# Kernel optimization log

Hardware: AMD Instinct MI355X
Metric: run time of the kernel (lower is better)

## Reference

```python
import jax, jax.numpy as jnp
import numpy as np

N_NODES = 50000
N_EDGES = 800000
IN_CH, HID, HEADS, OUT_CH = 16, 64, 4, 8
NEG_SLOPE = 0.2


def _add_self_loops(edge_index, num_nodes):
    loop = jnp.arange(num_nodes, dtype=edge_index.dtype)
    loops = jnp.stack([loop, loop])  # [2, N]
    return jnp.concatenate([edge_index, loops], axis=1)


def _gat_conv(x, src, dst, W, a_src, a_dst, bias, concat):
    """PyG-style GATConv: linear -> per-edge LeakyReLU attention -> segment
    softmax over incoming edges -> scatter-add aggregate."""
    N = x.shape[0]
    H, C = a_src.shape
    h = (x @ W).reshape(N, H, C)                      # [N,H,C]
    alpha_src = (h * a_src).sum(-1)                   # [N,H]
    alpha_dst = (h * a_dst).sum(-1)                   # [N,H]
    e = jax.nn.leaky_relu(alpha_src[src] + alpha_dst[dst], NEG_SLOPE)  # [E,H]
    # numerically stable segment softmax over edges grouped by dst
    e_max = jax.ops.segment_max(e, dst, num_segments=N)
    e_exp = jnp.exp(e - e_max[dst])
    denom = jax.ops.segment_sum(e_exp, dst, num_segments=N)
    alpha = e_exp / denom[dst]                        # [E,H]
    msg = h[src] * alpha[:, :, None]                  # [E,H,C]
    out = jax.ops.segment_sum(msg, dst, num_segments=N)  # [N,H,C]
    if concat:
        return out.reshape(N, H * C) + bias
    return out.mean(axis=1) + bias


def setup_inputs() -> dict:
    key = jax.random.key(0)
    ks = jax.random.split(key, 12)
    s = 0.1
    return {
        "x": jax.random.normal(ks[0], (N_NODES, IN_CH), jnp.float32),
        "edge_index": jax.random.randint(ks[1], (2, N_EDGES), 0, N_NODES, jnp.int64),
        "W1": jax.random.normal(ks[2], (IN_CH, HEADS * HID), jnp.float32) * s,
        "as1": jax.random.normal(ks[3], (HEADS, HID), jnp.float32) * s,
        "ad1": jax.random.normal(ks[4], (HEADS, HID), jnp.float32) * s,
        "b1": jnp.zeros((HEADS * HID,), jnp.float32),
        "W2": jax.random.normal(ks[5], (HEADS * HID, HEADS * HID), jnp.float32) * s,
        "as2": jax.random.normal(ks[6], (HEADS, HID), jnp.float32) * s,
        "ad2": jax.random.normal(ks[7], (HEADS, HID), jnp.float32) * s,
        "b2": jnp.zeros((HID,), jnp.float32),
        "Wc": jax.random.normal(ks[8], (HID, OUT_CH), jnp.float32) * s,
        "bc": jnp.zeros((OUT_CH,), jnp.float32),
    }


def reference(x, edge_index, W1, as1, ad1, b1, W2, as2, ad2, b2, Wc, bc):
    ei = _add_self_loops(edge_index, x.shape[0])
    src, dst = ei[0], ei[1]
    h = _gat_conv(x, src, dst, W1, as1, ad1, b1, concat=True)
    h = jax.nn.elu(h)
    h = _gat_conv(h, src, dst, W2, as2, ad2, b2, concat=False)
    h = jax.nn.elu(h)
    return h @ Wc + bc  # [N, OUT_CH]
```

## Files before the change

kernel.cpp:

```cpp
#include <hip/hip_runtime.h>
#include <math.h>

#define NODES   50000
#define HEADS   4
#define HID     64
#define FDIM    256
#define IN_CH   16
#define NEG_SLOPE 0.2f

typedef unsigned short ushort_t;
typedef unsigned int uint_t;
typedef __attribute__((ext_vector_type(8))) short bf16x8;
typedef __attribute__((ext_vector_type(4))) float f32x4;
typedef __attribute__((ext_vector_type(2))) float f32x2;

__device__ inline ushort_t f2bf(float f) {
    uint_t u = __float_as_uint(f);
    u += 0x7fffu + ((u >> 16) & 1u);
    return (ushort_t)(u >> 16);
}
__device__ inline uint_t f2h(float f) {
    _Float16 h = (_Float16)f;
    return (uint_t)*(ushort_t*)&h;
}
__device__ inline float h2f(uint_t u) {
    ushort_t us = (ushort_t)u;
    _Float16 h = *(_Float16*)&us;
    return (float)h;
}


__global__ __launch_bounds__(256) void k_prep(const float* __restrict__ x,
                                              const float* __restrict__ W1,
                                              const float* __restrict__ as1,
                                              const float* __restrict__ ad1,
                                              const float* __restrict__ W2,
                                              const int* __restrict__ ei, int E,
                                              ushort_t* __restrict__ h,
                                              float* __restrict__ asrc,
                                              float* __restrict__ adst,
                                              ushort_t* __restrict__ W2T,
                                              int* __restrict__ deg, int Nn, int NB) {
    int bid = blockIdx.x, t = threadIdx.x;
    if (bid >= NB + 256) {
        int e = (bid - NB - 256) * 256 + t;
        int Etot = E + Nn;
        if (e >= Etot) return;
        int d = (e < E) ? ei[E + e] : (e - E);
        if (d >= 0 && d < Nn) atomicAdd(&deg[d], 1);
        return;
    }
    if (bid >= NB) {
        int idx = (bid - NB) * 256 + t;
        int n = idx >> 8, k = idx & 255;
        W2T[idx] = f2bf(W2[k * FDIM + n]);
        return;
    }
    float w1c[16];
#pragma unroll
    for (int k = 0; k < 16; ++k) w1c[k] = W1[k * FDIM + t];
    float av = as1[t], dv = ad1[t];
    int hh = t >> 6;
#pragma unroll
    for (int j = 0; j < 8; ++j) {
        int n = bid * 8 + j;
        if (n >= Nn) break;
        const float4* xp = (const float4*)(x + n * IN_CH);
        float4 x0 = xp[0], x1 = xp[1], x2 = xp[2], x3 = xp[3];
        float s = x0.x * w1c[0]  + x0.y * w1c[1]  + x0.z * w1c[2]  + x0.w * w1c[3]
                + x1.x * w1c[4]  + x1.y * w1c[5]  + x1.z * w1c[6]  + x1.w * w1c[7]
                + x2.x * w1c[8]  + x2.y * w1c[9]  + x2.z * w1c[10] + x2.w * w1c[11]
                + x3.x * w1c[12] + x3.y * w1c[13] + x3.z * w1c[14] + x3.w * w1c[15];
        uint_t pv = (uint_t)f2bf(s);
        uint_t ov = __shfl_down(pv, 1);
        if (!(t & 1)) *(uint_t*)(h + (long)n * FDIM + t) = pv | (ov << 16);
        float p1 = s * av, p2 = s * dv;
#pragma unroll
        for (int off = 1; off < 64; off <<= 1) {
            p1 += __shfl_xor(p1, off);
            p2 += __shfl_xor(p2, off);
        }
        if ((t & 63) == 0) {
            asrc[n * 4 + hh] = p1;
            adst[n * 4 + hh] = p2;
        }
    }
}


__global__ __launch_bounds__(256) void k_scanA(const int* __restrict__ deg,
                                               int* __restrict__ bsum, int N) {
    __shared__ int sh[256];
    int t = threadIdx.x;
    int i0 = blockIdx.x * 4096 + t * 16;
    int s = 0;
#pragma unroll
    for (int j = 0; j < 16; ++j) s += (i0 + j < N) ? deg[i0 + j] : 0;
    sh[t] = s;
    __syncthreads();
    for (int off = 128; off; off >>= 1) {
        if (t < off) sh[t] += sh[t + off];
        __syncthreads();
    }
    if (t == 0) bsum[blockIdx.x] = sh[0];
}

__global__ void k_scanB(int* __restrict__ bsum, int* __restrict__ rowst, int nb, int N) {
    int t = threadIdx.x;
    int orig = (t < nb) ? bsum[t] : 0;
    int v = orig;
#pragma unroll
    for (int off = 1; off < 64; off <<= 1) {
        int u = __shfl_up(v, off);
        if (t >= off) v += u;
    }
    if (t < nb) bsum[t] = v - orig;
    if (t == 63) rowst[N] = v;
}

__global__ __launch_bounds__(256) void k_scanC(const int* __restrict__ deg,
                                               const int* __restrict__ bsum,
                                               int* __restrict__ rowst,
                                               int* __restrict__ cursor, int N) {
    __shared__ int sh[256];
    int t = threadIdx.x, b = blockIdx.x;
    int i0 = b * 4096 + t * 16;
    int v[16], s = 0;
#pragma unroll
    for (int j = 0; j < 16; ++j) { v[j] = (i0 + j < N) ? deg[i0 + j] : 0; s += v[j]; }
    sh[t] = s;
    __syncthreads();
    for (int off = 1; off < 256; off <<= 1) {
        int u = (t >= off) ? sh[t - off] : 0;
        __syncthreads();
        sh[t] += u;
        __syncthreads();
    }
    int excl = sh[t] - s + bsum[b];
#pragma unroll
    for (int j = 0; j < 16; ++j) {
        if (i0 + j < N) { rowst[i0 + j] = excl; cursor[i0 + j] = excl; }
        excl += v[j];
    }
}

__global__ void k_scatter(const int* __restrict__ ei, int E, int N,
                          int* __restrict__ cursor, int2* __restrict__ csr2) {
    int e = blockIdx.x * blockDim.x + threadIdx.x;
    int Etot = E + N;
    if (e >= Etot) return;
    int s, d;
    if (e < E) { s = ei[e]; d = ei[E + e]; } else { s = d = e - E; }
    if (d < 0 || d >= N) return;
    int pos = atomicAdd(&cursor[d], 1);
    csr2[pos] = make_int2(s, d);
}


__global__ __launch_bounds__(256) void k_gemm2(const ushort_t* __restrict__ A,
                                               const ushort_t* __restrict__ BT,
                                               const float* __restrict__ as2,
                                               const float* __restrict__ ad2,
                                               ushort_t* __restrict__ C,
                                               float* __restrict__ asrc,
                                               float* __restrict__ adst, int M) {
    __shared__ short As[64 * 40];
    __shared__ short Bs[64 * 40];
    __shared__ float2 red[64][2];
    int tid = threadIdx.x;
    int row0 = blockIdx.y * 64, col0 = blockIdx.x * 64;
    int wid = tid >> 6, lane = tid & 63;
    int wm = wid >> 1, wn = wid & 1;
    int quad = lane >> 4, lm = lane & 15;
    int lr = tid >> 2, lk = (tid & 3) * 8;
    f32x4 acc[2][2] = {};
    for (int k0 = 0; k0 < FDIM; k0 += 32) {
        uint4 av = {0u, 0u, 0u, 0u};
        int ar = row0 + lr;
        if (ar < M) av = *(const uint4*)(A + (long)ar * FDIM + k0 + lk);
        *(uint4*)(&As[lr * 40 + lk]) = av;
        uint4 bv = *(const uint4*)(BT + (long)(col0 + lr) * FDIM + k0 + lk);
        *(uint4*)(&Bs[lr * 40 + lk]) = bv;
        __syncthreads();
        bf16x8 a0 = *(const bf16x8*)(&As[(wm * 32 + lm) * 40 + quad * 8]);
        bf16x8 a1 = *(const bf16x8*)(&As[(wm * 32 + 16 + lm) * 40 + quad * 8]);
        bf16x8 b0 = *(const bf16x8*)(&Bs[(wn * 32 + lm) * 40 + quad * 8]);
        bf16x8 b1 = *(const bf16x8*)(&Bs[(wn * 32 + 16 + lm) * 40 + quad * 8]);
        acc[0][0] = __builtin_amdgcn_mfma_f32_16x16x32_bf16(a0, b0, acc[0][0], 0, 0, 0);
        acc[0][1] = __builtin_amdgcn_mfma_f32_16x16x32_bf16(a0, b1, acc[0][1], 0, 0, 0);
        acc[1][0] = __builtin_amdgcn_mfma_f32_16x16x32_bf16(a1, b0, acc[1][0], 0, 0, 0);
        acc[1][1] = __builtin_amdgcn_mfma_f32_16x16x32_bf16(a1, b1, acc[1][1], 0, 0, 0);
        __syncthreads();
    }
#pragma unroll
    for (int mi = 0; mi < 2; ++mi)
#pragma unroll
        for (int ni = 0; ni < 2; ++ni)
#pragma unroll
            for (int r = 0; r < 4; ++r) {
                int row = row0 + wm * 32 + mi * 16 + quad * 4 + r;
                int col = col0 + wn * 32 + ni * 16 + lm;
                if (row < M) C[(long)row * FDIM + col] = f2bf(acc[mi][ni][r]);
            }
    float asv0 = as2[col0 + wn * 32 + lm], asv1 = as2[col0 + wn * 32 + 16 + lm];
    float adv0 = ad2[col0 + wn * 32 + lm], adv1 = ad2[col0 + wn * 32 + 16 + lm];
#pragma unroll
    for (int mi = 0; mi < 2; ++mi)
#pragma unroll
        for (int r = 0; r < 4; ++r) {
            float ps = acc[mi][0][r] * asv0 + acc[mi][1][r] * asv1;
            float pd = acc[mi][0][r] * adv0 + acc[mi][1][r] * adv1;
#pragma unroll
            for (int off = 1; off < 16; off <<= 1) {
                ps += __shfl_xor(ps, off);
                pd += __shfl_xor(pd, off);
            }
            if (lm == 0) red[wm * 32 + mi * 16 + quad * 4 + r][wn] = make_float2(ps, pd);
        }
    __syncthreads();
    if (tid < 64) {
        int row = row0 + tid;
        if (row < M) {
            float2 e0 = red[tid][0], e1 = red[tid][1];
            asrc[row * 4 + blockIdx.x] = e0.x + e1.x;
            adst[row * 4 + blockIdx.x] = e0.y + e1.y;
        }
    }
}


__global__ void k_pw(const int2* __restrict__ csr2, const float* __restrict__ asrc,
                     const float* __restrict__ adst, uint_t* __restrict__ pwb, int Etot) {
    int e = blockIdx.x * blockDim.x + threadIdx.x;
    if (e >= Etot) return;
    int2 sd = csr2[e];
    float4 av = *(const float4*)(asrc + sd.x * 4);
    float4 dv = *(const float4*)(adst + sd.y * 4);
    float t[4] = {av.x + dv.x, av.y + dv.y, av.z + dv.z, av.w + dv.w};
    uint_t sh = (uint_t)sd.x << 16;
#pragma unroll
    for (int h = 0; h < 4; ++h) {
        float tt = (t[h] > 0.f) ? t[h] : NEG_SLOPE * t[h];
        pwb[h * Etot + e] = sh | f2h(__expf(tt));
    }
}


__device__ inline void fma8(f32x2& a0, f32x2& a1, f32x2& a2, f32x2& a3,
                            uint4 hv, float pw) {
    f32x2 p = {pw, pw};
    f32x2 u;
    u.x = __uint_as_float(hv.x << 16); u.y = __uint_as_float(hv.x & 0xffff0000u);
    a0 += p * u;
    u.x = __uint_as_float(hv.y << 16); u.y = __uint_as_float(hv.y & 0xffff0000u);
    a1 += p * u;
    u.x = __uint_as_float(hv.z << 16); u.y = __uint_as_float(hv.z & 0xffff0000u);
    a2 += p * u;
    u.x = __uint_as_float(hv.w << 16); u.y = __uint_as_float(hv.w & 0xffff0000u);
    a3 += p * u;
}

__global__ __launch_bounds__(256) void k_agg(const ushort_t* __restrict__ h,
                                             const uint_t* __restrict__ pwb,
                                             const int* __restrict__ row_start,
                                             const float* __restrict__ b1,
                                             const float* __restrict__ b2,
                                             const float* __restrict__ Wc,
                                             const float* __restrict__ bc,
                                             ushort_t* __restrict__ hout,
                                             float* __restrict__ fout,
                                             int mode, int Etot, int N) {
    __shared__ float zsh[2 * FDIM];
    __shared__ float wsh[584];
    int tid  = threadIdx.x;
    int hh   = tid >> 6;
    int lane = tid & 63;
    int half = lane >> 5;
    int l32  = lane & 31;
    int g    = l32 >> 3;
    int cg   = l32 & 7;
    int d    = blockIdx.x * 2 + half;
    bool valid = d < N;

    if (!mode) {
        for (int i = tid; i < 584; i += 256)
            wsh[i] = (i < 512) ? Wc[i] : ((i < 520) ? bc[i - 512] : b2[i - 520]);
    }

    int s0 = 0, s1 = 0;
    if (valid) { s0 = row_start[d]; s1 = row_start[d + 1]; }
    int cnt  = s1 - s0;
    int maxc = max(cnt, __shfl_xor(cnt, 32));
    const uint_t* pwp = pwb + (long)hh * Etot;
    const char* hbase = (const char*)h + (hh * HID + cg * 8) * 2;

    f32x2 a0 = {0.f, 0.f}, a1 = {0.f, 0.f}, a2 = {0.f, 0.f}, a3 = {0.f, 0.f};
    float den = 0.f;

    for (int off = 0; off < maxc; off += 16) {
        int i0 = s0 + off + g;
        uint_t u0 = (i0      < s1) ? pwp[i0]      : 0u;
        uint_t u1 = (i0 + 4  < s1) ? pwp[i0 + 4]  : 0u;
        uint_t u2 = (i0 + 8  < s1) ? pwp[i0 + 8]  : 0u;
        uint_t u3 = (i0 + 12 < s1) ? pwp[i0 + 12] : 0u;
        uint4 hv0 = *(const uint4*)(hbase + ((size_t)(u0 >> 16) << 9));
        uint4 hv1 = *(const uint4*)(hbase + ((size_t)(u1 >> 16) << 9));
        uint4 hv2 = *(const uint4*)(hbase + ((size_t)(u2 >> 16) << 9));
        uint4 hv3 = *(const uint4*)(hbase + ((size_t)(u3 >> 16) << 9));
        float pw0 = h2f(u0 & 0xffffu), pw1 = h2f(u1 & 0xffffu);
        float pw2 = h2f(u2 & 0xffffu), pw3 = h2f(u3 & 0xffffu);
        den += (pw0 + pw1) + (pw2 + pw3);
        fma8(a0, a1, a2, a3, hv0, pw0);
        fma8(a0, a1, a2, a3, hv1, pw1);
        fma8(a0, a1, a2, a3, hv2, pw2);
        fma8(a0, a1, a2, a3, hv3, pw3);
    }
#pragma unroll
    for (int off = 8; off <= 16; off <<= 1) {
        a0.x += __shfl_xor(a0.x, off); a0.y += __shfl_xor(a0.y, off);
        a1.x += __shfl_xor(a1.x, off); a1.y += __shfl_xor(a1.y, off);
        a2.x += __shfl_xor(a2.x, off); a2.y += __shfl_xor(a2.y, off);
        a3.x += __shfl_xor(a3.x, off); a3.y += __shfl_xor(a3.y, off);
        den  += __shfl_xor(den, off);
    }

    if (mode) {
        if (g == 0 && valid) {
            float inv = 1.f / den;
            float v[8] = {a0.x, a0.y, a1.x, a1.y, a2.x, a2.y, a3.x, a3.y};
            const float* bp = b1 + hh * HID + cg * 8;
#pragma unroll
            for (int j = 0; j < 8; ++j) {
                float t = v[j] * inv + bp[j];
                v[j] = (t > 0.f) ? t : __expf(t) - 1.f;
            }
            uint4 u;
            u.x = (uint_t)f2bf(v[0]) | ((uint_t)f2bf(v[1]) << 16);
            u.y = (uint_t)f2bf(v[2]) | ((uint_t)f2bf(v[3]) << 16);
            u.z = (uint_t)f2bf(v[4]) | ((uint_t)f2bf(v[5]) << 16);
            u.w = (uint_t)f2bf(v[6]) | ((uint_t)f2bf(v[7]) << 16);
            *(uint4*)(hout + (long)d * FDIM + hh * HID + cg * 8) = u;
        }
    } else {
        if (g == 0 && valid) {
            float inv = 1.f / den;
            float v[8] = {a0.x, a0.y, a1.x, a1.y, a2.x, a2.y, a3.x, a3.y};
            int zb = half * FDIM + hh * HID + cg * 8;
#pragma unroll
            for (int j = 0; j < 8; ++j) zsh[zb + j] = v[j] * inv;
        }
        __syncthreads();
        if (tid < 128) {
            int node = tid >> 6, c = tid & 63;
            int dd = blockIdx.x * 2 + node;
            if (dd < N) {
                const float* zp = zsh + node * FDIM;
                float zv = 0.25f * (zp[c] + zp[64 + c] + zp[128 + c] + zp[192 + c])
                         + wsh[520 + c];
                zv = (zv > 0.f) ? zv : __expf(zv) - 1.f;
                zsh[node * FDIM + c] = zv;
            }
        }
        __syncthreads();
        if (tid < 16) {
            int node = tid >> 3, o = tid & 7;
            int dd = blockIdx.x * 2 + node;
            if (dd < N) {
                float acc = wsh[512 + o];
                const float* zp = zsh + node * FDIM;
#pragma unroll 8
                for (int c = 0; c < 64; ++c) acc += zp[c] * wsh[c * 8 + o];
                fout[(long)dd * 8 + o] = acc;
            }
        }
    }
}


extern "C" void kernel_launch(void* const* d_in, const int* in_sizes, int n_in,
                              void* d_out, int out_size, void* d_ws, size_t ws_size,
                              hipStream_t stream) {
    const float* x   = (const float*)d_in[0];
    const int*   ei  = (const int*)d_in[1];
    const float* W1  = (const float*)d_in[2];
    const float* as1 = (const float*)d_in[3];
    const float* ad1 = (const float*)d_in[4];
    const float* b1  = (const float*)d_in[5];
    const float* W2  = (const float*)d_in[6];
    const float* as2 = (const float*)d_in[7];
    const float* ad2 = (const float*)d_in[8];
    const float* b2  = (const float*)d_in[9];
    const float* Wc  = (const float*)d_in[10];
    const float* bc  = (const float*)d_in[11];
    float* out = (float*)d_out;

    const int N = NODES;
    const int E = in_sizes[1] / 2;
    const int Etot = E + N;

    char* ws = (char*)d_ws;
    size_t off = 0;
    auto alloc = [&](size_t bytes) {
        void* p = ws + off;
        off = (off + bytes + 255) & ~(size_t)255;
        return p;
    };
    ushort_t* hbf    = (ushort_t*)alloc((size_t)N * FDIM * 2);
    ushort_t* hact   = (ushort_t*)alloc((size_t)N * FDIM * 2);
    float*    asrc   = (float*)alloc((size_t)N * HEADS * 4);
    float*    adst   = (float*)alloc((size_t)N * HEADS * 4);
    ushort_t* W2T    = (ushort_t*)alloc((size_t)FDIM * FDIM * 2);
    int*      deg    = (int*)alloc((size_t)N * 4);
    int*      rowst  = (int*)alloc((size_t)(N + 1) * 4);
    int*      cursor = (int*)alloc((size_t)N * 4);
    int*      bsum   = (int*)alloc(64 * 4);
    int2*     csr2   = (int2*)alloc((size_t)Etot * 8);
    uint_t*   pwb    = (uint_t*)alloc((size_t)Etot * HEADS * 4);

    const int tpb = 256;
    int egrid = (Etot + tpb - 1) / tpb;
    int nb = (N + 4095) / 4096;
    int NB = (N + 7) / 8;

    hipMemsetAsync(deg, 0, (size_t)N * 4, stream);

    k_prep<<<NB + 256 + egrid, tpb, 0, stream>>>(x, W1, as1, ad1, W2, ei, E,
                                                 hbf, asrc, adst, W2T, deg, N, NB);
    k_scanA<<<nb, 256, 0, stream>>>(deg, bsum, N);
    k_scanB<<<1, 64, 0, stream>>>(bsum, rowst, nb, N);
    k_scanC<<<nb, 256, 0, stream>>>(deg, bsum, rowst, cursor, N);
    k_scatter<<<egrid, tpb, 0, stream>>>(ei, E, N, cursor, csr2);

    k_pw<<<egrid, tpb, 0, stream>>>(csr2, asrc, adst, pwb, Etot);
    k_agg<<<(N + 1) / 2, 256, 0, stream>>>(hbf, pwb, rowst, b1, nullptr, nullptr, nullptr,
                                           hact, nullptr, 1, Etot, N);

    dim3 g2(FDIM / 64, (N + 63) / 64);
    k_gemm2<<<g2, 256, 0, stream>>>(hact, W2T, as2, ad2, hbf, asrc, adst, N);
    k_pw<<<egrid, tpb, 0, stream>>>(csr2, asrc, adst, pwb, Etot);
    k_agg<<<(N + 1) / 2, 256, 0, stream>>>(hbf, pwb, rowst, nullptr, b2, Wc, bc,
                                           nullptr, out, 0, Etot, N);
}
```

Measured before the change: 380.1 us.

## Widen GEMM2 tile to full 256 columns and fold scanB into scanC

The layer-2 GEMM now gives each block 64 rows and all 256 output columns. Each wave owns one head's 64 columns, so the attention logits are reduced inside the wave and written directly, with no shared-memory reduction and no extra barrier. The A tile is loaded once per row block instead of four times, at the cost of a larger B tile in shared memory, more accumulator registers and a quarter as many blocks. Separately, the single-block scanB kernel is removed: every scanC block recomputes the block-offset prefix itself, which saves one kernel launch.

```diff
diff --git a/kernel.cpp b/kernel.cpp
--- a/kernel.cpp
+++ b/kernel.cpp
@@ -105,25 +105,24 @@
     if (t == 0) bsum[blockIdx.x] = sh[0];
 }
 
-__global__ void k_scanB(int* __restrict__ bsum, int* __restrict__ rowst, int nb, int N) {
-    int t = threadIdx.x;
-    int orig = (t < nb) ? bsum[t] : 0;
-    int v = orig;
-#pragma unroll
-    for (int off = 1; off < 64; off <<= 1) {
-        int u = __shfl_up(v, off);
-        if (t >= off) v += u;
-    }
-    if (t < nb) bsum[t] = v - orig;
-    if (t == 63) rowst[N] = v;
-}
-
 __global__ __launch_bounds__(256) void k_scanC(const int* __restrict__ deg,
                                                const int* __restrict__ bsum,
                                                int* __restrict__ rowst,
-                                               int* __restrict__ cursor, int N) {
+                                               int* __restrict__ cursor, int N, int nb) {
     __shared__ int sh[256];
+    __shared__ int boff[64];
     int t = threadIdx.x, b = blockIdx.x;
+    if (t < 64) {
+        int orig = (t < nb) ? bsum[t] : 0;
+        int v = orig;
+#pragma unroll
+        for (int off = 1; off < 64; off <<= 1) {
+            int u = __shfl_up(v, off);
+            if (t >= off) v += u;
+        }
+        boff[t] = v - orig;
+        if (t == 63 && b == 0) rowst[N] = v;
+    }
     int i0 = b * 4096 + t * 16;
     int v[16], s = 0;
 #pragma unroll
@@ -136,7 +135,7 @@
         sh[t] += u;
         __syncthreads();
     }
-    int excl = sh[t] - s + bsum[b];
+    int excl = sh[t] - s + boff[b];
 #pragma unroll
     for (int j = 0; j < 16; ++j) {
         if (i0 + j < N) { rowst[i0 + j] = excl; cursor[i0 + j] = excl; }
@@ -165,67 +164,76 @@
                                                float* __restrict__ asrc,
                                                float* __restrict__ adst, int M) {
     __shared__ short As[64 * 40];
-    __shared__ short Bs[64 * 40];
-    __shared__ float2 red[64][2];
+    __shared__ short Bs[256 * 40];
     int tid = threadIdx.x;
-    int row0 = blockIdx.y * 64, col0 = blockIdx.x * 64;
-    int wid = tid >> 6, lane = tid & 63;
-    int wm = wid >> 1, wn = wid & 1;
+    int row0 = blockIdx.x * 64;
+    int w = tid >> 6, lane = tid & 63;
     int quad = lane >> 4, lm = lane & 15;
     int lr = tid >> 2, lk = (tid & 3) * 8;
-    f32x4 acc[2][2] = {};
+    f32x4 acc[4][4] = {};
     for (int k0 = 0; k0 < FDIM; k0 += 32) {
         uint4 av = {0u, 0u, 0u, 0u};
         int ar = row0 + lr;
         if (ar < M) av = *(const uint4*)(A + (long)ar * FDIM + k0 + lk);
         *(uint4*)(&As[lr * 40 + lk]) = av;
-        uint4 bv = *(const uint4*)(BT + (long)(col0 + lr) * FDIM + k0 + lk);
-        *(uint4*)(&Bs[lr * 40 + lk]) = bv;
-        __syncthreads();
-        bf16x8 a0 = *(const bf16x8*)(&As[(wm * 32 + lm) * 40 + quad * 8]);
-        bf16x8 a1 = *(const bf16x8*)(&As[(wm * 32 + 16 + lm) * 40 + quad * 8]);
-        bf16x8 b0 = *(const bf16x8*)(&Bs[(wn * 32 + lm) * 40 + quad * 8]);
-        bf16x8 b1 = *(const bf16x8*)(&Bs[(wn * 32 + 16 + lm) * 40 + quad * 8]);
-        acc[0][0] = __builtin_amdgcn_mfma_f32_16x16x32_bf16(a0, b0, acc[0][0], 0, 0, 0);
-        acc[0][1] = __builtin_amdgcn_mfma_f32_16x16x32_bf16(a0, b1, acc[0][1], 0, 0, 0);
-        acc[1][0] = __builtin_amdgcn_mfma_f32_16x16x32_bf16(a1, b0, acc[1][0], 0, 0, 0);
-        acc[1][1] = __builtin_amdgcn_mfma_f32_16x16x32_bf16(a1, b1, acc[1][1], 0, 0, 0);
-        __syncthreads();
-    }
-#pragma unroll
-    for (int mi = 0; mi < 2; ++mi)
-#pragma unroll
-        for (int ni = 0; ni < 2; ++ni)
+#pragma unroll
+        for (int seg = 0; seg < 4; ++seg) {
+            int n = seg * 64 + lr;
+            uint4 bv = *(const uint4*)(BT + (long)n * FDIM + k0 + lk);
+            *(uint4*)(&Bs[n * 40 + lk]) = bv;
+        }
+        __syncthreads();
+        bf16x8 af[4], bf[4];
+#pragma unroll
+        for (int i = 0; i < 4; ++i) {
+            af[i] = *(const bf16x8*)(&As[(i * 16 + lm) * 40 + quad * 8]);
+            bf[i] = *(const bf16x8*)(&Bs[(w * 64 + i * 16 + lm) * 40 + quad * 8]);
+        }
+#pragma unroll
+        for (int mi = 0; mi < 4; ++mi)
+#pragma unroll
+            for (int ni = 0; ni < 4; ++ni)
+                acc[mi][ni] = __builtin_amdgcn_mfma_f32_16x16x32_bf16(af[mi], bf[ni],
+                                                                      acc[mi][ni], 0, 0, 0);
+        __syncthreads();
+    }
+#pragma unroll
+    for (int mi = 0; mi < 4; ++mi)
+#pragma unroll
+        for (int ni = 0; ni < 4; ++ni)
 #pragma unroll
             for (int r = 0; r < 4; ++r) {
-                int row = row0 + wm * 32 + mi * 16 + quad * 4 + r;
-                int col = col0 + wn * 32 + ni * 16 + lm;
-                if (row < M) C[(long)row * FDIM + col] = f2bf(acc[mi][ni][r]);
-            }
-    float asv0 = as2[col0 + wn * 32 + lm], asv1 = as2[col0 + wn * 32 + 16 + lm];
-    float adv0 = ad2[col0 + wn * 32 + lm], adv1 = ad2[col0 + wn * 32 + 16 + lm];
-#pragma unroll
-    for (int mi = 0; mi < 2; ++mi)
+                int row = row0 + mi * 16 + quad * 4 + r;
+                if (row < M)
+                    C[(long)row * FDIM + w * 64 + ni * 16 + lm] = f2bf(acc[mi][ni][r]);
+            }
+    float asv[4], adv[4];
+#pragma unroll
+    for (int ni = 0; ni < 4; ++ni) {
+        asv[ni] = as2[w * 64 + ni * 16 + lm];
+        adv[ni] = ad2[w * 64 + ni * 16 + lm];
+    }
+#pragma unroll
+    for (int mi = 0; mi < 4; ++mi)
 #pragma unroll
         for (int r = 0; r < 4; ++r) {
-            float ps = acc[mi][0][r] * asv0 + acc[mi][1][r] * asv1;
-            float pd = acc[mi][0][r] * adv0 + acc[mi][1][r] * adv1;
+            float ps = acc[mi][0][r] * asv[0] + acc[mi][1][r] * asv[1]
+                     + acc[mi][2][r] * asv[2] + acc[mi][3][r] * asv[3];
+            float pd = acc[mi][0][r] * adv[0] + acc[mi][1][r] * adv[1]
+                     + acc[mi][2][r] * adv[2] + acc[mi][3][r] * adv[3];
 #pragma unroll
             for (int off = 1; off < 16; off <<= 1) {
                 ps += __shfl_xor(ps, off);
                 pd += __shfl_xor(pd, off);
             }
-            if (lm == 0) red[wm * 32 + mi * 16 + quad * 4 + r][wn] = make_float2(ps, pd);
-        }
-    __syncthreads();
-    if (tid < 64) {
-        int row = row0 + tid;
-        if (row < M) {
-            float2 e0 = red[tid][0], e1 = red[tid][1];
-            asrc[row * 4 + blockIdx.x] = e0.x + e1.x;
-            adst[row * 4 + blockIdx.x] = e0.y + e1.y;
-        }
-    }
+            if (lm == 0) {
+                int row = row0 + mi * 16 + quad * 4 + r;
+                if (row < M) {
+                    asrc[row * 4 + w] = ps;
+                    adst[row * 4 + w] = pd;
+                }
+            }
+        }
 }
 
 
@@ -427,16 +435,14 @@
     k_prep<<<NB + 256 + egrid, tpb, 0, stream>>>(x, W1, as1, ad1, W2, ei, E,
                                                  hbf, asrc, adst, W2T, deg, N, NB);
     k_scanA<<<nb, 256, 0, stream>>>(deg, bsum, N);
-    k_scanB<<<1, 64, 0, stream>>>(bsum, rowst, nb, N);
-    k_scanC<<<nb, 256, 0, stream>>>(deg, bsum, rowst, cursor, N);
+    k_scanC<<<nb, 256, 0, stream>>>(deg, bsum, rowst, cursor, N, nb);
     k_scatter<<<egrid, tpb, 0, stream>>>(ei, E, N, cursor, csr2);
 
     k_pw<<<egrid, tpb, 0, stream>>>(csr2, asrc, adst, pwb, Etot);
     k_agg<<<(N + 1) / 2, 256, 0, stream>>>(hbf, pwb, rowst, b1, nullptr, nullptr, nullptr,
                                            hact, nullptr, 1, Etot, N);
 
-    dim3 g2(FDIM / 64, (N + 63) / 64);
-    k_gemm2<<<g2, 256, 0, stream>>>(hact, W2T, as2, ad2, hbf, asrc, adst, N);
+    k_gemm2<<<(N + 63) / 64, 256, 0, stream>>>(hact, W2T, as2, ad2, hbf, asrc, adst, N);
     k_pw<<<egrid, tpb, 0, stream>>>(csr2, asrc, adst, pwb, Etot);
     k_agg<<<(N + 1) / 2, 256, 0, stream>>>(hbf, pwb, rowst, nullptr, b2, Wc, bc,
                                            nullptr, out, 0, Etot, N);
```

New measurement: 386.2 us. Within noise of the previous version (+1.6%).

## Fuse scan offsets into scanC, attention weights into scatter, add agg tail loop

Applied to the files above, without the earlier changes.

Merges the block-offset scan into the final scan kernel, so one launch disappears. The first layer's per-edge attention-weight computation moves into the CSR scatter kernel, which drops a separate pass over the edges. The aggregation loop gains a 4-edge remainder loop so low-degree nodes stop wasting masked loads. The cost is that each scanC block redundantly recomputes the small prefix over the block sums.

```diff
diff --git a/kernel.cpp b/kernel.cpp
--- a/kernel.cpp
+++ b/kernel.cpp
@@ -105,25 +105,24 @@
     if (t == 0) bsum[blockIdx.x] = sh[0];
 }
 
-__global__ void k_scanB(int* __restrict__ bsum, int* __restrict__ rowst, int nb, int N) {
-    int t = threadIdx.x;
-    int orig = (t < nb) ? bsum[t] : 0;
-    int v = orig;
-#pragma unroll
-    for (int off = 1; off < 64; off <<= 1) {
-        int u = __shfl_up(v, off);
-        if (t >= off) v += u;
-    }
-    if (t < nb) bsum[t] = v - orig;
-    if (t == 63) rowst[N] = v;
-}
-
 __global__ __launch_bounds__(256) void k_scanC(const int* __restrict__ deg,
                                                const int* __restrict__ bsum,
                                                int* __restrict__ rowst,
-                                               int* __restrict__ cursor, int N) {
+                                               int* __restrict__ cursor, int N, int nb) {
     __shared__ int sh[256];
+    __shared__ int boff[64];
     int t = threadIdx.x, b = blockIdx.x;
+    if (t < 64) {
+        int orig = (t < nb) ? bsum[t] : 0;
+        int v = orig;
+#pragma unroll
+        for (int off = 1; off < 64; off <<= 1) {
+            int u = __shfl_up(v, off);
+            if (t >= off) v += u;
+        }
+        boff[t] = v - orig;
+        if (t == 63 && b == 0) rowst[N] = v;
+    }
     int i0 = b * 4096 + t * 16;
     int v[16], s = 0;
 #pragma unroll
@@ -136,7 +135,7 @@
         sh[t] += u;
         __syncthreads();
     }
-    int excl = sh[t] - s + bsum[b];
+    int excl = sh[t] - s + boff[b];
 #pragma unroll
     for (int j = 0; j < 16; ++j) {
         if (i0 + j < N) { rowst[i0 + j] = excl; cursor[i0 + j] = excl; }
@@ -144,16 +143,27 @@
     }
 }
 
+
 __global__ void k_scatter(const int* __restrict__ ei, int E, int N,
-                          int* __restrict__ cursor, int2* __restrict__ csr2) {
+                          int* __restrict__ cursor, int2* __restrict__ csr2,
+                          const float* __restrict__ asrc, const float* __restrict__ adst,
+                          uint_t* __restrict__ pwb, int Etot) {
     int e = blockIdx.x * blockDim.x + threadIdx.x;
-    int Etot = E + N;
     if (e >= Etot) return;
     int s, d;
     if (e < E) { s = ei[e]; d = ei[E + e]; } else { s = d = e - E; }
     if (d < 0 || d >= N) return;
     int pos = atomicAdd(&cursor[d], 1);
     csr2[pos] = make_int2(s, d);
+    float4 av = *(const float4*)(asrc + s * 4);
+    float4 dv = *(const float4*)(adst + d * 4);
+    float tt[4] = {av.x + dv.x, av.y + dv.y, av.z + dv.z, av.w + dv.w};
+    uint_t sh = (uint_t)s << 16;
+#pragma unroll
+    for (int h = 0; h < 4; ++h) {
+        float v = (tt[h] > 0.f) ? tt[h] : NEG_SLOPE * tt[h];
+        pwb[h * Etot + pos] = sh | f2h(__expf(v));
+    }
 }
 
 
@@ -291,13 +301,15 @@
     if (valid) { s0 = row_start[d]; s1 = row_start[d + 1]; }
     int cnt  = s1 - s0;
     int maxc = max(cnt, __shfl_xor(cnt, 32));
+    int mend = maxc & ~15;
     const uint_t* pwp = pwb + (long)hh * Etot;
     const char* hbase = (const char*)h + (hh * HID + cg * 8) * 2;
 
     f32x2 a0 = {0.f, 0.f}, a1 = {0.f, 0.f}, a2 = {0.f, 0.f}, a3 = {0.f, 0.f};
     float den = 0.f;
-
-    for (int off = 0; off < maxc; off += 16) {
+    int off = 0;
+
+    for (; off < mend; off += 16) {
         int i0 = s0 + off + g;
         uint_t u0 = (i0      < s1) ? pwp[i0]      : 0u;
         uint_t u1 = (i0 + 4  < s1) ? pwp[i0 + 4]  : 0u;
@@ -315,13 +327,21 @@
         fma8(a0, a1, a2, a3, hv2, pw2);
         fma8(a0, a1, a2, a3, hv3, pw3);
     }
-#pragma unroll
-    for (int off = 8; off <= 16; off <<= 1) {
-        a0.x += __shfl_xor(a0.x, off); a0.y += __shfl_xor(a0.y, off);
-        a1.x += __shfl_xor(a1.x, off); a1.y += __shfl_xor(a1.y, off);
-        a2.x += __shfl_xor(a2.x, off); a2.y += __shfl_xor(a2.y, off);
-        a3.x += __shfl_xor(a3.x, off); a3.y += __shfl_xor(a3.y, off);
-        den  += __shfl_xor(den, off);
+    for (; off < maxc; off += 4) {
+        int i0 = s0 + off + g;
+        uint_t u0 = (i0 < s1) ? pwp[i0] : 0u;
+        uint4 hv0 = *(const uint4*)(hbase + ((size_t)(u0 >> 16) << 9));
+        float pw0 = h2f(u0 & 0xffffu);
+        den += pw0;
+        fma8(a0, a1, a2, a3, hv0, pw0);
+    }
+#pragma unroll
+    for (int o = 8; o <= 16; o <<= 1) {
+        a0.x += __shfl_xor(a0.x, o); a0.y += __shfl_xor(a0.y, o);
+        a1.x += __shfl_xor(a1.x, o); a1.y += __shfl_xor(a1.y, o);
+        a2.x += __shfl_xor(a2.x, o); a2.y += __shfl_xor(a2.y, o);
+        a3.x += __shfl_xor(a3.x, o); a3.y += __shfl_xor(a3.y, o);
+        den  += __shfl_xor(den, o);
     }
 
     if (mode) {
@@ -427,11 +447,9 @@
     k_prep<<<NB + 256 + egrid, tpb, 0, stream>>>(x, W1, as1, ad1, W2, ei, E,
                                                  hbf, asrc, adst, W2T, deg, N, NB);
     k_scanA<<<nb, 256, 0, stream>>>(deg, bsum, N);
-    k_scanB<<<1, 64, 0, stream>>>(bsum, rowst, nb, N);
-    k_scanC<<<nb, 256, 0, stream>>>(deg, bsum, rowst, cursor, N);
-    k_scatter<<<egrid, tpb, 0, stream>>>(ei, E, N, cursor, csr2);
-
-    k_pw<<<egrid, tpb, 0, stream>>>(csr2, asrc, adst, pwb, Etot);
+    k_scanC<<<nb, 256, 0, stream>>>(deg, bsum, rowst, cursor, N, nb);
+    k_scatter<<<egrid, tpb, 0, stream>>>(ei, E, N, cursor, csr2, asrc, adst, pwb, Etot);
+
     k_agg<<<(N + 1) / 2, 256, 0, stream>>>(hbf, pwb, rowst, b1, nullptr, nullptr, nullptr,
                                            hact, nullptr, 1, Etot, N);
 
```

Measured after the change: 394.3 us. 1.04x slower.
